# Performance work log

Measured on AMD Instinct MI355X. Metric: run time of the kernel, lower is better.

Reference implementation:

```python
import jax, jax.numpy as jnp
import numpy as np
from jax import lax

# --- module constants (from init_kwargs) ---
A_COEF = 0.7
B_COEF = 0.0
RADIUS = 8
EPS = 1e-3
EPS_LOG = 1e-6
EPS_SCALE = 1e-4
DOWN = 0.5
KSIZE = 2 * RADIUS + 1


def _sep_box_filter(x4):
    """Separable box filter on [1,1,H,W] with reflect padding (matches torch)."""
    p = jnp.pad(x4, ((0, 0), (0, 0), (RADIUS, RADIUS), (RADIUS, RADIUS)), mode='reflect')
    box_h = jnp.full((1, 1, 1, KSIZE), 1.0 / KSIZE, dtype=x4.dtype)
    box_v = jnp.full((1, 1, KSIZE, 1), 1.0 / KSIZE, dtype=x4.dtype)
    h = lax.conv(p, box_h, (1, 1), 'VALID')
    return lax.conv(h, box_v, (1, 1), 'VALID')


def _guided_filter(I2d):
    """Self-guided filter on [H,W] (guide == input)."""
    I4 = I2d[None, None]
    mean_I = _sep_box_filter(I4)
    mean_II = _sep_box_filter(I4 * I4)
    var_I = mean_II - mean_I * mean_I
    a = var_I / (var_I + EPS)
    b = mean_I - a * mean_I
    mean_a = _sep_box_filter(a)
    mean_b = _sep_box_filter(b)
    out = mean_a * I4 + mean_b
    return out[0, 0]


def _resize_bilinear(img, out_h, out_w):
    """Bilinear resize of [H,W], torch align_corners=False semantics (no antialias)."""
    in_h, in_w = img.shape
    ys = jnp.clip((jnp.arange(out_h, dtype=jnp.float32) + 0.5) * (in_h / out_h) - 0.5,
                  0.0, in_h - 1.0)
    xs = jnp.clip((jnp.arange(out_w, dtype=jnp.float32) + 0.5) * (in_w / out_w) - 0.5,
                  0.0, in_w - 1.0)
    y0 = jnp.floor(ys).astype(jnp.int32)
    x0 = jnp.floor(xs).astype(jnp.int32)
    y1 = jnp.minimum(y0 + 1, in_h - 1)
    x1 = jnp.minimum(x0 + 1, in_w - 1)
    wy = (ys - y0)[:, None]  # [out_h,1]
    wx = (xs - x0)[None, :]  # [1,out_w]
    Ia = img[y0][:, x0]
    Ib = img[y0][:, x1]
    Ic = img[y1][:, x0]
    Id = img[y1][:, x1]
    top = Ia * (1.0 - wx) + Ib * wx
    bot = Ic * (1.0 - wx) + Id * wx
    return top * (1.0 - wy) + bot * wy


def setup_inputs() -> dict:
    key = jax.random.key(0)
    x = jax.random.uniform(key, (2160, 3840, 3), dtype=jnp.float32)  # RGB in [0,1]
    return {"x": x}


def reference(x) -> jnp.ndarray:
    H, W = x.shape[0], x.shape[1]
    R, G, B = x[..., 0], x[..., 1], x[..., 2]
    Y = 0.2126 * R + 0.7152 * G + 0.0722 * B
    Y_log = jnp.log2(jnp.maximum(Y, EPS_LOG))

    # downsample -> guided filter -> upsample (DOWN < 1.0 path)
    dh, dw = int(H * DOWN), int(W * DOWN)
    Y_log_down = _resize_bilinear(Y_log, dh, dw)
    Y_base_down = _guided_filter(Y_log_down)
    Y_base = _resize_bilinear(Y_base_down, H, W)

    Y_detail = Y_log - Y_base
    Y_tm = (A_COEF * Y_base + B_COEF) + Y_detail
    Y_out = jnp.exp2(Y_tm)
    scale = Y_out / (Y + EPS_SCALE)
    out = x * scale[..., None]
    return jnp.clip(out, 0.0, 1.0)
```

## Files before the change

### kernel.cpp

```cpp
#include <hip/hip_runtime.h>

#define FH 2160
#define FW 3840
#define DH 1080
#define DW 1920
#define RAD 8
#define KS 17
#define INV_KS (1.0f / 17.0f)
#define EPS_GF 1e-3f
#define EPS_LOG 1e-6f
#define EPS_SCALE 1e-4f
#define A_COEF 0.7f

#define TS 32
#define IT 48
#define ITP 49

#define AT 50
#define ATP 51
#define BT 34
#define BTP 35

#define NTILES 2040
#define TPX 255

__device__ __forceinline__ int refl(int p, int n) {
    p = (p < 0) ? -p : p;
    return (p >= n) ? (2 * n - 2 - p) : p;
}

__device__ __forceinline__ float luma3(float r, float g, float b) {
    return 0.2126f * r + 0.7152f * g + 0.0722f * b;
}

__global__ void __launch_bounds__(256, 4)
k_gf_front(const float* __restrict__ x, float* __restrict__ Dg,
           float* __restrict__ Ag, float* __restrict__ Bg) {
    __shared__ float inD[IT * ITP];
    __shared__ float h1[IT * TS];
    __shared__ float h2[IT * TS];
    int bid = blockIdx.x;
    int swz = (bid & 7) * TPX + (bid >> 3);
    int bx = swz % 60, by = swz / 60;
    int tx0 = bx * TS, ty0 = by * TS;
    int t = threadIdx.x;

    for (int s = t; s < IT * IT; s += 256) {
        int li = s / IT, lj = s - li * IT;
        int gi = refl(ty0 - RAD + li, DH);
        int gj = refl(tx0 - RAD + lj, DW);
        const float* p0 = x + ((size_t)(2 * gi) * FW + (size_t)(2 * gj)) * 3;
        const float* p1 = p0 + (size_t)FW * 3;
        float2 a0 = *(const float2*)(p0);
        float2 a1 = *(const float2*)(p0 + 2);
        float2 a2 = *(const float2*)(p0 + 4);
        float2 b0 = *(const float2*)(p1);
        float2 b1 = *(const float2*)(p1 + 2);
        float2 b2 = *(const float2*)(p1 + 4);
        float y00 = luma3(a0.x, a0.y, a1.x);
        float y01 = luma3(a1.y, a2.x, a2.y);
        float y10 = luma3(b0.x, b0.y, b1.x);
        float y11 = luma3(b1.y, b2.x, b2.y);
        inD[li * ITP + lj] = 0.25f * (__log2f(fmaxf(y00, EPS_LOG)) +
                                      __log2f(fmaxf(y01, EPS_LOG)) +
                                      __log2f(fmaxf(y10, EPS_LOG)) +
                                      __log2f(fmaxf(y11, EPS_LOG)));
    }
    __syncthreads();

    for (int idx = t; idx < IT * TS; idx += 256) {
        int r = idx >> 5, c = idx & 31;
        const float* row = &inD[r * ITP + c];
        float s1 = 0.f, s2 = 0.f;
#pragma unroll
        for (int k = 0; k < KS; ++k) { float v = row[k]; s1 += v; s2 += v * v; }
        h1[idx] = s1 * INV_KS;
        h2[idx] = s2 * INV_KS;
    }
    __syncthreads();

    for (int idx = t; idx < TS * TS; idx += 256) {
        int r = idx >> 5, c = idx & 31;
        int gi = ty0 + r;
        if (gi < DH) {
            float s1 = 0.f, s2 = 0.f;
#pragma unroll
            for (int k = 0; k < KS; ++k) {
                s1 += h1[(r + k) * TS + c];
                s2 += h2[(r + k) * TS + c];
            }
            float mI = s1 * INV_KS, mII = s2 * INV_KS;
            float var = mII - mI * mI;
            float av = var / (var + EPS_GF);
            size_t g = (size_t)gi * DW + tx0 + c;
            Ag[g] = av;
            Bg[g] = mI - av * mI;
            Dg[g] = inD[(r + RAD) * ITP + c + RAD];
        }
    }
}

__global__ void __launch_bounds__(256)
k_gf_back(const float* __restrict__ x, const float* __restrict__ Ag,
          const float* __restrict__ Bg, const float* __restrict__ Dg,
          float* __restrict__ out) {
    __shared__ float inA[AT * ATP];
    __shared__ float inB[AT * ATP];
    __shared__ float hA[AT * BT];
    __shared__ float hB[AT * BT];
    __shared__ float baseT[BT * BTP];
    int bid = blockIdx.x;
    int swz = (bid & 7) * TPX + (bid >> 3);
    int bx = swz % 60, by = swz / 60;
    int ox0 = bx * 64, oy0 = by * 64;
    int bh0 = by * 32 - 1, bw0 = bx * 32 - 1;
    int ah0 = bh0 - RAD, aw0 = bw0 - RAD;
    int t = threadIdx.x;

    for (int s = t; s < AT * AT; s += 256) {
        int li = s / AT, lj = s - li * AT;
        size_t g = (size_t)refl(ah0 + li, DH) * DW + refl(aw0 + lj, DW);
        inA[li * ATP + lj] = Ag[g];
        inB[li * ATP + lj] = Bg[g];
    }
    __syncthreads();

    for (int idx = t; idx < AT * BT; idx += 256) {
        int r = idx / BT, c = idx - r * BT;
        const float* ra = &inA[r * ATP + c];
        const float* rb = &inB[r * ATP + c];
        float s1 = 0.f, s2 = 0.f;
#pragma unroll
        for (int k = 0; k < KS; ++k) { s1 += ra[k]; s2 += rb[k]; }
        hA[r * BT + c] = s1 * INV_KS;
        hB[r * BT + c] = s2 * INV_KS;
    }
    __syncthreads();

    for (int idx = t; idx < BT * BT; idx += 256) {
        int r = idx / BT, c = idx - r * BT;
        float s1 = 0.f, s2 = 0.f;
#pragma unroll
        for (int k = 0; k < KS; ++k) {
            s1 += hA[(r + k) * BT + c];
            s2 += hB[(r + k) * BT + c];
        }
        size_t g = (size_t)refl(bh0 + r, DH) * DW + refl(bw0 + c, DW);
        baseT[r * BTP + c] = (s1 * INV_KS) * Dg[g] + s2 * INV_KS;
    }
    __syncthreads();

    for (int q = t; q < 64 * 16; q += 256) {
        int qi = q >> 4, qj = q & 15;
        int oy = oy0 + qi;
        if (oy < FH) {
            float ys = fminf(fmaxf((oy + 0.5f) * 0.5f - 0.5f, 0.f), (float)(DH - 1));
            int y0 = (int)ys;
            int y1 = min(y0 + 1, DH - 1);
            float wy = ys - (float)y0;
            const float* br0 = &baseT[(y0 - bh0) * BTP];
            const float* br1 = &baseT[(y1 - bh0) * BTP];

            size_t off = ((size_t)oy * FW + (size_t)(ox0 + 4 * qj)) * 3;
            const float4* xin = (const float4*)(x + off);
            float4 v0 = xin[0], v1 = xin[1], v2 = xin[2];
            float px[12] = {v0.x, v0.y, v0.z, v0.w, v1.x, v1.y, v1.z, v1.w,
                            v2.x, v2.y, v2.z, v2.w};
            float po[12];
#pragma unroll
            for (int p = 0; p < 4; ++p) {
                int ox = ox0 + 4 * qj + p;
                float xs = fminf(fmaxf((ox + 0.5f) * 0.5f - 0.5f, 0.f), (float)(DW - 1));
                int x0 = (int)xs;
                int x1 = min(x0 + 1, DW - 1);
                float wx = xs - (float)x0;
                int c0 = x0 - bw0, c1 = x1 - bw0;
                float top = br0[c0] * (1.f - wx) + br0[c1] * wx;
                float bot = br1[c0] * (1.f - wx) + br1[c1] * wx;
                float Yb = top * (1.f - wy) + bot * wy;

                float cr = px[3 * p], cg = px[3 * p + 1], cb = px[3 * p + 2];
                float Y = luma3(cr, cg, cb);
                float Ylog = __log2f(fmaxf(Y, EPS_LOG));
                float Yout = exp2f(A_COEF * Yb + (Ylog - Yb));
                float sc = Yout / (Y + EPS_SCALE);
                po[3 * p + 0] = fminf(fmaxf(cr * sc, 0.f), 1.f);
                po[3 * p + 1] = fminf(fmaxf(cg * sc, 0.f), 1.f);
                po[3 * p + 2] = fminf(fmaxf(cb * sc, 0.f), 1.f);
            }
            float4* op = (float4*)(out + off);
            op[0] = make_float4(po[0], po[1], po[2], po[3]);
            op[1] = make_float4(po[4], po[5], po[6], po[7]);
            op[2] = make_float4(po[8], po[9], po[10], po[11]);
        }
    }
}

extern "C" void kernel_launch(void* const* d_in, const int* in_sizes, int n_in,
                              void* d_out, int out_size, void* d_ws, size_t ws_size,
                              hipStream_t stream) {
    const float* x = (const float*)d_in[0];
    float* out = (float*)d_out;
    float* ws = (float*)d_ws;
    const size_t DN = (size_t)DW * DH;

    float* D = ws;
    float* A = ws + DN;
    float* B = ws + 2 * DN;

    k_gf_front<<<dim3(NTILES), dim3(256), 0, stream>>>(x, D, A, B);
    k_gf_back <<<dim3(NTILES), dim3(256), 0, stream>>>(x, A, B, D, out);
}
```

Baseline: 77.12 us.

## Fuse guided-filter front and back kernels into one tile kernel with halo recompute

Merges the two-kernel pipeline into a single kernel. Each 64x64 output tile builds a 66x66 downsampled log-luma halo, computes the a/b coefficients over a 50x50 region, then box-filters them and upsamples, all in shared memory. This removes the global round trip of the D, A and B intermediates and one kernel launch. In exchange it recomputes overlapping halo work: each tile reads more of the input x and does more box-filter arithmetic. It also uses more LDS per block, which lowers the occupancy bound to 3.

```diff
diff --git a/kernel.cpp b/kernel.cpp
--- a/kernel.cpp
+++ b/kernel.cpp
@@ -12,10 +12,8 @@
 #define EPS_SCALE 1e-4f
 #define A_COEF 0.7f
 
-#define TS 32
-#define IT 48
-#define ITP 49
-
+#define DT 66
+#define DTP 67
 #define AT 50
 #define ATP 51
 #define BT 34
@@ -33,22 +31,25 @@
     return 0.2126f * r + 0.7152f * g + 0.0722f * b;
 }
 
-__global__ void __launch_bounds__(256, 4)
-k_gf_front(const float* __restrict__ x, float* __restrict__ Dg,
-           float* __restrict__ Ag, float* __restrict__ Bg) {
-    __shared__ float inD[IT * ITP];
-    __shared__ float h1[IT * TS];
-    __shared__ float h2[IT * TS];
+__global__ void __launch_bounds__(256, 3)
+k_ltm(const float* __restrict__ x, float* __restrict__ out) {
+    __shared__ float R0[5100];
+    __shared__ float R1[6600];
+    __shared__ float R2[1156];
+
     int bid = blockIdx.x;
     int swz = (bid & 7) * TPX + (bid >> 3);
     int bx = swz % 60, by = swz / 60;
-    int tx0 = bx * TS, ty0 = by * TS;
+    int ox0 = bx * 64, oy0 = by * 64;
+    int bh0 = by * 32 - 1, bw0 = bx * 32 - 1;
+    int dh0 = bh0 - 2 * RAD, dw0 = bw0 - 2 * RAD;
     int t = threadIdx.x;
 
-    for (int s = t; s < IT * IT; s += 256) {
-        int li = s / IT, lj = s - li * IT;
-        int gi = refl(ty0 - RAD + li, DH);
-        int gj = refl(tx0 - RAD + lj, DW);
+    float* inD = R0;
+    for (int s = t; s < DT * DT; s += 256) {
+        int li = s / DT, lj = s - li * DT;
+        int gi = refl(dh0 + li, DH);
+        int gj = refl(dw0 + lj, DW);
         const float* p0 = x + ((size_t)(2 * gi) * FW + (size_t)(2 * gj)) * 3;
         const float* p1 = p0 + (size_t)FW * 3;
         float2 a0 = *(const float2*)(p0);
@@ -61,70 +62,50 @@
         float y01 = luma3(a1.y, a2.x, a2.y);
         float y10 = luma3(b0.x, b0.y, b1.x);
         float y11 = luma3(b1.y, b2.x, b2.y);
-        inD[li * ITP + lj] = 0.25f * (__log2f(fmaxf(y00, EPS_LOG)) +
+        inD[li * DTP + lj] = 0.25f * (__log2f(fmaxf(y00, EPS_LOG)) +
                                       __log2f(fmaxf(y01, EPS_LOG)) +
                                       __log2f(fmaxf(y10, EPS_LOG)) +
                                       __log2f(fmaxf(y11, EPS_LOG)));
     }
     __syncthreads();
 
-    for (int idx = t; idx < IT * TS; idx += 256) {
-        int r = idx >> 5, c = idx & 31;
-        const float* row = &inD[r * ITP + c];
+    float* h1 = R1;
+    float* h2 = R1 + 3300;
+    for (int idx = t; idx < DT * AT; idx += 256) {
+        int r = idx / AT, c = idx - r * AT;
+        const float* row = &inD[r * DTP + c];
         float s1 = 0.f, s2 = 0.f;
 #pragma unroll
         for (int k = 0; k < KS; ++k) { float v = row[k]; s1 += v; s2 += v * v; }
         h1[idx] = s1 * INV_KS;
         h2[idx] = s2 * INV_KS;
     }
-    __syncthreads();
-
-    for (int idx = t; idx < TS * TS; idx += 256) {
-        int r = idx >> 5, c = idx & 31;
-        int gi = ty0 + r;
-        if (gi < DH) {
-            float s1 = 0.f, s2 = 0.f;
-#pragma unroll
-            for (int k = 0; k < KS; ++k) {
-                s1 += h1[(r + k) * TS + c];
-                s2 += h2[(r + k) * TS + c];
-            }
-            float mI = s1 * INV_KS, mII = s2 * INV_KS;
-            float var = mII - mI * mI;
-            float av = var / (var + EPS_GF);
-            size_t g = (size_t)gi * DW + tx0 + c;
-            Ag[g] = av;
-            Bg[g] = mI - av * mI;
-            Dg[g] = inD[(r + RAD) * ITP + c + RAD];
-        }
-    }
-}
-
-__global__ void __launch_bounds__(256)
-k_gf_back(const float* __restrict__ x, const float* __restrict__ Ag,
-          const float* __restrict__ Bg, const float* __restrict__ Dg,
-          float* __restrict__ out) {
-    __shared__ float inA[AT * ATP];
-    __shared__ float inB[AT * ATP];
-    __shared__ float hA[AT * BT];
-    __shared__ float hB[AT * BT];
-    __shared__ float baseT[BT * BTP];
-    int bid = blockIdx.x;
-    int swz = (bid & 7) * TPX + (bid >> 3);
-    int bx = swz % 60, by = swz / 60;
-    int ox0 = bx * 64, oy0 = by * 64;
-    int bh0 = by * 32 - 1, bw0 = bx * 32 - 1;
-    int ah0 = bh0 - RAD, aw0 = bw0 - RAD;
-    int t = threadIdx.x;
-
-    for (int s = t; s < AT * AT; s += 256) {
-        int li = s / AT, lj = s - li * AT;
-        size_t g = (size_t)refl(ah0 + li, DH) * DW + refl(aw0 + lj, DW);
-        inA[li * ATP + lj] = Ag[g];
-        inB[li * ATP + lj] = Bg[g];
+    for (int idx = t; idx < BT * BT; idx += 256) {
+        int r = idx / BT, c = idx - r * BT;
+        R2[idx] = inD[(r + 2 * RAD) * DTP + (c + 2 * RAD)];
     }
     __syncthreads();
 
+    float* inA = R0;
+    float* inB = R0 + 2550;
+    for (int idx = t; idx < AT * AT; idx += 256) {
+        int r = idx / AT, c = idx - r * AT;
+        float s1 = 0.f, s2 = 0.f;
+#pragma unroll
+        for (int k = 0; k < KS; ++k) {
+            s1 += h1[(r + k) * AT + c];
+            s2 += h2[(r + k) * AT + c];
+        }
+        float mI = s1 * INV_KS, mII = s2 * INV_KS;
+        float var = mII - mI * mI;
+        float av = var / (var + EPS_GF);
+        inA[r * ATP + c] = av;
+        inB[r * ATP + c] = mI - av * mI;
+    }
+    __syncthreads();
+
+    float* hA = R1;
+    float* hB = R1 + 3300;
     for (int idx = t; idx < AT * BT; idx += 256) {
         int r = idx / BT, c = idx - r * BT;
         const float* ra = &inA[r * ATP + c];
@@ -137,6 +118,7 @@
     }
     __syncthreads();
 
+    float* baseT = R1 + 5000;
     for (int idx = t; idx < BT * BT; idx += 256) {
         int r = idx / BT, c = idx - r * BT;
         float s1 = 0.f, s2 = 0.f;
@@ -145,8 +127,7 @@
             s1 += hA[(r + k) * BT + c];
             s2 += hB[(r + k) * BT + c];
         }
-        size_t g = (size_t)refl(bh0 + r, DH) * DW + refl(bw0 + c, DW);
-        baseT[r * BTP + c] = (s1 * INV_KS) * Dg[g] + s2 * INV_KS;
+        baseT[r * BTP + c] = (s1 * INV_KS) * R2[idx] + s2 * INV_KS;
     }
     __syncthreads();
 
@@ -201,13 +182,5 @@
                               hipStream_t stream) {
     const float* x = (const float*)d_in[0];
     float* out = (float*)d_out;
-    float* ws = (float*)d_ws;
-    const size_t DN = (size_t)DW * DH;
-
-    float* D = ws;
-    float* A = ws + DN;
-    float* B = ws + 2 * DN;
-
-    k_gf_front<<<dim3(NTILES), dim3(256), 0, stream>>>(x, D, A, B);
-    k_gf_back <<<dim3(NTILES), dim3(256), 0, stream>>>(x, A, B, D, out);
+    k_ltm<<<dim3(NTILES), dim3(256), 0, stream>>>(x, out);
 }
```

Result: slower. 91.21 us (+18.3%).
